# Kernel optimization log

Hardware: AMD Instinct MI355X
Metric: run time of the kernel (lower is better)

Reference implementation:

```python
import jax, jax.numpy as jnp
import numpy as np

B, N, L = 32, 50, 16384  # batch, n_templates, segment length
KT = 4096                # template kernel length


def conv1d(x, w, pad, groups=1):
    # x: [B, Cin, L], w: [Cout, Cin/groups, K] (torch layout)
    return jax.lax.conv_general_dilated(
        x, w, window_strides=(1,), padding=[(pad, pad)],
        dimension_numbers=('NCH', 'OIH', 'NCH'), feature_group_count=groups)


def maxpool3(x):
    # MaxPool1d(kernel=3, stride=3), floor mode (VALID)
    return jax.lax.reduce_window(x, -jnp.inf, jax.lax.max,
                                 (1, 1, 3), (1, 1, 3), 'VALID')


def pad_to(x, m):
    p = (-x.shape[-1]) % m
    pads = ((0, 0),) * (x.ndim - 1) + ((0, p),)
    return jnp.pad(x, pads)


def setup_inputs() -> dict:
    key = jax.random.key(0)
    ks = jax.random.split(key, 12)
    return dict(
        xi=jax.random.normal(ks[0], (B, 2, L), jnp.float32),
        S_t_m12=jax.random.normal(ks[1], (2, 1, L), jnp.float32) * 0.01,
        template=jax.random.normal(ks[2], (N, 2, KT), jnp.float32) * 0.01,
        hh_sqrt=jax.random.uniform(ks[3], (N, 2), jnp.float32) + 0.5,
        W1=jax.random.normal(ks[4], (16, 2, 3), jnp.float32) * 0.1,
        b1=jnp.zeros((16,), jnp.float32),
        W2=jax.random.normal(ks[5], (32, 16, 3), jnp.float32) * 0.1,
        b2=jnp.zeros((32,), jnp.float32),
        W3=jax.random.normal(ks[6], (32, 128), jnp.float32) * 0.1,
        b3=jnp.zeros((32,), jnp.float32),
        W4=jax.random.normal(ks[7], (2, 32), jnp.float32) * 0.1,
        b4=jnp.zeros((2,), jnp.float32),
    )


def reference(xi, S_t_m12, template, hh_sqrt, W1, b1, W2, b2, W3, b3, W4, b4):
    # Whitening matched filter: grouped conv with kernel length L
    y = conv1d(xi, S_t_m12, L - 1, groups=2)          # [B, 2, 2L-1]
    y = pad_to(y, L)                                   # [B, 2, 2L]
    # wrap-fold each channel: reshape(B,2,L).sum over the fold axis
    d_SA = y[:, 0].reshape(-1, 2, L).sum(1)[:, None, :]  # [B,1,L]
    d_SE = y[:, 1].reshape(-1, 2, L).sum(1)[:, None, :]
    h_SA = template[:, 0, :].reshape(-1, 1, KT)          # [N,1,KT]
    h_SE = template[:, 1, :].reshape(-1, 1, KT)
    dh_A = pad_to(conv1d(d_SA, h_SA, KT - 1), L).reshape(-1, N, 2, L).sum(2)  # [B,N,L]
    dh_E = pad_to(conv1d(d_SE, h_SE, KT - 1), L).reshape(-1, N, 2, L).sum(2)
    z = jnp.stack((dh_A, dh_E), -1).transpose(0, 2, 1, 3)  # [B,L,N,2]
    z = z / hh_sqrt                                         # broadcast [N,2]
    z = z.max(axis=1).transpose(0, 2, 1)                    # [B,2,N]
    # small CNN + MLP head
    h = maxpool3(jax.nn.sigmoid(conv1d(z, W1, 0) + b1[None, :, None]))  # [B,16,16]
    h = maxpool3(jax.nn.sigmoid(conv1d(h, W2, 0) + b2[None, :, None]))  # [B,32,4]
    h = h.reshape(h.shape[0], -1)                                        # [B,128]
    h = jax.nn.relu(h @ W3.T + b3)
    return h @ W4.T + b4                                                 # [B,2]
```

## Files before the change

kernel.cpp:

```cpp
#include <hip/hip_runtime.h>
#include <math.h>

#define L_LEN 16384
#define M_LEN 8192
#define KT_LEN 4096
#define BB 32
#define NTPL 50
#define SPEC_STRIDE 8224
#define NSIG 166
#define NTI 512
#define PI_F 3.14159265358979323846f
#define R2_F 0.70710678118654752f
#define CW1 0.99999970586288223f
#define SW1 7.6699031874270453e-4f

typedef float cf2 __attribute__((ext_vector_type(2)));


__device__ __forceinline__ cf2 cmul(cf2 a, cf2 b) {
    cf2 t, d;
    asm("v_pk_mul_f32 %0, %1, %2 op_sel:[0,0] op_sel_hi:[0,1]"
        : "=v"(t) : "v"(a), "v"(b));
    asm("v_pk_fma_f32 %0, %1, %2, %3 op_sel:[1,1,0] op_sel_hi:[1,0,1] neg_lo:[0,1,0]"
        : "=v"(d) : "v"(a), "v"(b), "v"(t));
    return d;
}
__device__ __forceinline__ cf2 cmulc(cf2 a, cf2 b) {
    cf2 t, d;
    asm("v_pk_mul_f32 %0, %1, %2 op_sel:[0,0] op_sel_hi:[0,1] neg_hi:[0,1]"
        : "=v"(t) : "v"(a), "v"(b));
    asm("v_pk_fma_f32 %0, %1, %2, %3 op_sel:[1,1,0] op_sel_hi:[1,0,1]"
        : "=v"(d) : "v"(a), "v"(b), "v"(t));
    return d;
}
__device__ __forceinline__ cf2 cmulca(cf2 a, cf2 b) {
    cf2 t, d;
    asm("v_pk_mul_f32 %0, %1, %2 op_sel:[0,0] op_sel_hi:[0,1]"
        : "=v"(t) : "v"(a), "v"(b));
    asm("v_pk_fma_f32 %0, %1, %2, %3 op_sel:[1,1,0] op_sel_hi:[1,0,1] neg_hi:[1,0,0]"
        : "=v"(d) : "v"(a), "v"(b), "v"(t));
    return d;
}
__device__ __forceinline__ cf2 pk_addch(cf2 a, cf2 b) {
    cf2 d;
    asm("v_pk_add_f32 %0, %1, %2 neg_hi:[0,1]" : "=v"(d) : "v"(a), "v"(b));
    return d;
}
__device__ __forceinline__ cf2 pk_subcl(cf2 a, cf2 b) {
    cf2 d;
    asm("v_pk_add_f32 %0, %1, %2 neg_lo:[0,1]" : "=v"(d) : "v"(a), "v"(b));
    return d;
}
__device__ __forceinline__ cf2 pk_compose1(cf2 s, cf2 r) {
    cf2 d;
    asm("v_pk_add_f32 %0, %1, %2 op_sel:[0,1] op_sel_hi:[0,0] neg_lo:[0,1]"
        : "=v"(d) : "v"(s), "v"(r));
    return d;
}
__device__ __forceinline__ cf2 pk_compose2(cf2 s, cf2 r) {
    cf2 d;
    asm("v_pk_add_f32 %0, %1, %2 op_sel:[0,1] op_sel_hi:[0,0] neg_hi:[1,0]"
        : "=v"(d) : "v"(s), "v"(r));
    return d;
}
template<int SIGN>
__device__ __forceinline__ cf2 rot90(cf2 z) {
    return (SIGN < 0) ? (cf2){z.y, -z.x} : (cf2){-z.y, z.x};
}
template<int SIGN>
__device__ __forceinline__ cf2 ldT(const cf2* __restrict__ T, int idx) {
    cf2 t = T[idx];
    if (SIGN > 0) t.y = -t.y;
    return t;
}

__device__ __forceinline__ int swz(int i) { return i ^ (((i >> 5) & 15) << 1); }

__device__ __forceinline__ int pos4(int f) {
    return ((f & 15) << 8) | (f & 0xF0) | ((f >> 8) & 15);
}

template<int SIGN>
__device__ __forceinline__ void dft16(cf2 x[16]) {
    const float S = (SIGN < 0) ? -1.f : 1.f;
    const cf2 w1 = {0.9238795325112867f, S * 0.3826834323650898f};
    const cf2 w2 = {0.7071067811865476f, S * 0.7071067811865476f};
    const cf2 w3 = {0.3826834323650898f, S * 0.9238795325112867f};
    cf2 v[16];
    #pragma unroll
    for (int n1 = 0; n1 < 4; ++n1) {
        cf2 a0 = x[n1], a1 = x[n1+4], a2 = x[n1+8], a3 = x[n1+12];
        cf2 t0 = a0 + a2, t2 = a0 - a2;
        cf2 t1 = a1 + a3, t3 = rot90<SIGN>(a1 - a3);
        cf2 u0 = t0 + t1, u1 = t2 + t3;
        cf2 u2 = t0 - t1, u3 = t2 - t3;
        if (n1 == 1) { u1 = cmul(u1, w1); u2 = cmul(u2, w2); u3 = cmul(u3, w3); }
        else if (n1 == 2) { u1 = cmul(u1, w2); u2 = rot90<SIGN>(u2);
                            u3 = rot90<SIGN>(cmul(u3, w2)); }
        else if (n1 == 3) { u1 = cmul(u1, w3); u2 = rot90<SIGN>(cmul(u2, w2));
                            u3 = -cmul(u3, w1); }
        v[0*4+n1] = u0; v[1*4+n1] = u1; v[2*4+n1] = u2; v[3*4+n1] = u3;
    }
    #pragma unroll
    for (int r = 0; r < 4; ++r) {
        cf2 a0 = v[r*4+0], a1 = v[r*4+1], a2 = v[r*4+2], a3 = v[r*4+3];
        cf2 t0 = a0 + a2, t2 = a0 - a2;
        cf2 t1 = a1 + a3, t3 = rot90<SIGN>(a1 - a3);
        x[r]    = t0 + t1; x[r+4]  = t2 + t3;
        x[r+8]  = t0 - t1; x[r+12] = t2 - t3;
    }
}

template<int SIGN>
__device__ __forceinline__ void butterfly16(cf2* A, const int idx[16], cf2 w1) {
    cf2 x[16];
    #pragma unroll
    for (int n = 0; n < 16; ++n) x[n] = A[idx[n]];
    dft16<SIGN>(x);
    A[idx[0]] = x[0];
    A[idx[1]] = cmul(x[1], w1);
    const cf2 w2 = cmul(w1, w1);
    A[idx[2]] = cmul(x[2], w2);
    const cf2 w3 = cmul(w1, w2);
    A[idx[3]] = cmul(x[3], w3);
    const cf2 w4 = cmul(w2, w2);
    A[idx[4]] = cmul(x[4], w4);
    A[idx[5]] = cmul(x[5], cmul(w1, w4));
    A[idx[6]] = cmul(x[6], cmul(w2, w4));
    A[idx[7]] = cmul(x[7], cmul(w3, w4));
    const cf2 w8 = cmul(w4, w4);
    A[idx[8]]  = cmul(x[8],  w8);
    A[idx[9]]  = cmul(x[9],  cmul(w1, w8));
    A[idx[10]] = cmul(x[10], cmul(w2, w8));
    A[idx[11]] = cmul(x[11], cmul(w3, w8));
    const cf2 w12 = cmul(w4, w8);
    A[idx[12]] = cmul(x[12], w12);
    A[idx[13]] = cmul(x[13], cmul(w1, w12));
    A[idx[14]] = cmul(x[14], cmul(w2, w12));
    A[idx[15]] = cmul(x[15], cmul(w3, w12));
}

__global__ __launch_bounds__(256, 4)
void fwd_fft_kernel(const float* __restrict__ xi, const float* __restrict__ w,
                    const float* __restrict__ tmpl, cf2* __restrict__ Tw,
                    cf2* __restrict__ spec) {
    __shared__ __attribute__((aligned(16))) cf2 A[4096];
    const int hb = blockIdx.x;
    const int tid = threadIdx.x;

    if (hb >= 2*NSIG) {
        const int k = (hb - 2*NSIG) * 256 + tid;
        const int quad = k >> 12, mm = k & 4095;
        float s, c; __sincosf(PI_F * (float)mm / 8192.f, &s, &c);
        cf2 v;
        if      (quad == 0) v = (cf2){ c, -s};
        else if (quad == 1) v = (cf2){-s, -c};
        else if (quad == 2) v = (cf2){-c,  s};
        else                v = (cf2){ s,  c};
        Tw[k] = v;
        return;
    }

    const int sig = hb >> 1, half = hb & 1;
    const float* src;
    int nre;
    if (sig < 64)      { src = xi   + sig * L_LEN;         nre = L_LEN; }
    else if (sig < 66) { src = w    + (sig - 64) * L_LEN;  nre = L_LEN; }
    else               { src = tmpl + (sig - 66) * KT_LEN; nre = KT_LEN; }
    const bool isW = (sig >= 64 && sig < 66);
    const int nf4 = nre >> 2;
    const float4* s4 = (const float4*)src;

    const cf2 w1c = (cf2){CW1, -SW1};
    #pragma unroll
    for (int mm = 0; mm < 8; ++mm) {
        const int j = tid + 256*mm;
        float4 a = (j < nf4)        ? s4[j]        : make_float4(0.f,0.f,0.f,0.f);
        float4 b = (j + 2048 < nf4) ? s4[j + 2048] : make_float4(0.f,0.f,0.f,0.f);
        cf2 c0 = (cf2){a.x, a.y}, c1 = (cf2){a.z, a.w};
        cf2 d0 = (cf2){b.x, b.y}, d1 = (cf2){b.z, b.w};
        cf2 h0, h1;
        if (half == 0) { h0 = c0 + d0; h1 = c1 + d1; }
        else {
            float sn, cs; __sincosf(-PI_F * (float)j / 2048.f, &sn, &cs);
            cf2 wk = (cf2){cs, sn};
            h0 = cmul(c0 - d0, wk);
            h1 = cmul(c1 - d1, cmul(wk, w1c));
        }
        const int g = j ^ ((j >> 4) & 15);
        ((float4*)A)[g] = make_float4(h0.x, h0.y, h1.x, h1.y);
    }
    __syncthreads();

    {
        const int jx = tid ^ (((tid >> 5) & 7) << 1);
        int idx[16];
        #pragma unroll
        for (int n = 0; n < 16; ++n) idx[n] = (jx ^ ((n & 1) << 4)) + 256*n;
        float sn, cs; __sincosf(-PI_F * (float)tid / 2048.f, &sn, &cs);
        butterfly16<-1>(A, idx, (cf2){cs, sn});
    }
    __syncthreads();
    {
        const int q = tid >> 4, j = tid & 15;
        const int base = q << 8, qb = q & 1;
        int idx[16];
        #pragma unroll
        for (int n = 0; n < 16; ++n)
            idx[n] = base + 16*(n ^ qb) + (j ^ (((n >> 1) & 7) << 1));
        float sn, cs; __sincosf(-PI_F * (float)j / 128.f, &sn, &cs);
        butterfly16<-1>(A, idx, (cf2){cs, sn});
    }
    __syncthreads();
    {
        const int bb = 16 * (tid ^ ((tid >> 4) & 1));
        const int m3 = ((tid >> 1) & 7) << 1;
        cf2 x[16];
        #pragma unroll
        for (int e = 0; e < 8; ++e) {
            float4 v = ((const float4*)A)[(bb + ((2*e) ^ m3)) >> 1];
            x[2*e]     = (cf2){v.x, v.y};
            x[2*e + 1] = (cf2){v.z, v.w};
        }
        dft16<-1>(x);
        #pragma unroll
        for (int e = 0; e < 8; ++e)
            ((float4*)A)[(bb + ((2*e) ^ m3)) >> 1] =
                make_float4(x[2*e].x, x[2*e].y, x[2*e+1].x, x[2*e+1].y);
    }
    __syncthreads();

    cf2* out = spec + (size_t)sig * SPEC_STRIDE;
    #pragma unroll
    for (int mm = 0; mm < 16; ++mm) {
        const int m = tid + 256*mm;
        const int mb = half ? (4095 - m) : ((4096 - m) & 4095);
        const int f = 2*m + half;
        cf2 Za = A[swz(pos4(m))];
        cf2 Zb = A[swz(pos4(mb))];
        cf2 E = (cf2){0.5f*(Za.x + Zb.x), 0.5f*(Za.y - Zb.y)};
        cf2 D = (cf2){Za.x - Zb.x, Za.y + Zb.y};
        cf2 O = (cf2){0.5f*D.y, -0.5f*D.x};
        float sn, cs;
        __sincosf(-PI_F * (float)f / 8192.f, &sn, &cs);
        cf2 val = E + (cf2){cs*O.x - sn*O.y, cs*O.y + sn*O.x};
        if (isW) {
            const int k = (4094 * f) & (L_LEN - 1);
            float psn, pcs; __sincosf(-PI_F * (float)k / 8192.f, &psn, &pcs);
            val = cmul((cf2){val.x, -val.y}, (cf2){pcs, psn});
        }
        out[f] = val;
    }
    if (half == 0 && tid == 0) {
        cf2 Za = A[0];
        cf2 val = (cf2){Za.x - Za.y, 0.f};
        if (isW) {
            val = (cf2){-val.x, 0.f};
        }
        out[M_LEN] = val;
    }
}

__global__ __launch_bounds__(1024)
void xv_kernel(cf2* __restrict__ spec) {
    const int bc = blockIdx.x;
    cf2* Xs = spec + (size_t)bc * SPEC_STRIDE;
    const cf2* Vs = spec + (size_t)(64 + (bc & 1)) * SPEC_STRIDE;
    const int tid = threadIdx.x;
    float4* X4 = (float4*)Xs;
    const float4* V4 = (const float4*)Vs;
    #pragma unroll
    for (int m = 0; m < 4; ++m) {
        const int p = tid + 1024*m;
        float4 xv = X4[p], vv = V4[p];
        cf2 a = cmul((cf2){xv.x, xv.y}, (cf2){vv.x, vv.y});
        cf2 b = cmul((cf2){xv.z, xv.w}, (cf2){vv.z, vv.w});
        X4[p] = make_float4(a.x, a.y, b.x, b.y);
    }
    if (tid == 0) Xs[M_LEN] = cmul(Xs[M_LEN], Vs[M_LEN]);
}

__global__ __launch_bounds__(NTI, 4)
void inv_fft_kernel(const cf2* __restrict__ spec, const cf2* __restrict__ T,
                    const float* __restrict__ hh, float* __restrict__ zarr) {
    __shared__ __attribute__((aligned(16))) cf2 A[M_LEN];
    const int idx0 = blockIdx.x;
    const int c = idx0 & 1;
    const int n = (idx0 >> 1) % NTPL;
    const int b = idx0 / (2 * NTPL);
    const int tid = threadIdx.x;

    const cf2* Xs = spec + (size_t)(b*2 + c)      * SPEC_STRIDE;
    const cf2* Hs = spec + (size_t)(66 + n*2 + c) * SPEC_STRIDE;
    const float4* X4 = (const float4*)Xs;
    const float4* H4 = (const float4*)Hs;
    const float4* T4 = (const float4*)T;

    #pragma unroll
    for (int m = 0; m < 2; ++m) {
        const int tp = tid + 512*m;
        const int f0 = 2*tp, f1 = f0 + 1;
        float4 xa = X4[tp],        ha = H4[tp];
        float4 xq = X4[tp + 2048], hq = H4[tp + 2048];
        cf2 PA0 = cmulc((cf2){xa.x, xa.y}, (cf2){ha.x, ha.y});
        cf2 PA1 = cmulc((cf2){xa.z, xa.w}, (cf2){ha.z, ha.w});
        cf2 QB0 = cmulc((cf2){xq.x, xq.y}, (cf2){hq.x, hq.y});
        cf2 QB1 = cmulc((cf2){xq.z, xq.w}, (cf2){hq.z, hq.w});
        cf2 PB0 = cmulc(Xs[4096 - f0], Hs[4096 - f0]);
        cf2 PB1 = cmulc(Xs[4096 - f1], Hs[4096 - f1]);
        cf2 QA0 = cmulc(Xs[8192 - f0], Hs[8192 - f0]);
        cf2 QA1 = cmulc(Xs[8192 - f1], Hs[8192 - f1]);
        float4 tf4 = T4[tp];
        float4 t2a = T4[2*tp];
        float4 t2b = T4[2*tp + 1];
        cf2 Tf0 = (cf2){tf4.x, tf4.y}, Tf1 = (cf2){tf4.z, tf4.w};
        cf2 T20 = (cf2){t2a.x, t2a.y}, T21 = (cf2){t2b.x, t2b.y};
        cf2 SpA0 = pk_addch(PA0, QA0), SmA0 = pk_subcl(PA0, QA0);
        cf2 RA0 = cmulca(Tf0, SmA0);
        cf2 ZA1_0 = pk_compose1(SpA0, RA0);
        cf2 ZA2_0 = pk_compose2(SpA0, RA0);
        cf2 tB0 = (cf2){-Tf0.y, -Tf0.x};
        cf2 SpB0 = pk_addch(PB0, QB0), SmB0 = pk_subcl(PB0, QB0);
        cf2 RB0 = cmulca(tB0, SmB0);
        cf2 ZB1_0 = pk_compose1(SpB0, RB0);
        cf2 ZB2_0 = pk_compose2(SpB0, RB0);
        cf2 top0 = ZA1_0 + ZB2_0;
        cf2 bot0 = cmulca(T20, ZA1_0 - ZB2_0);
        cf2 SpA1 = pk_addch(PA1, QA1), SmA1 = pk_subcl(PA1, QA1);
        cf2 RA1 = cmulca(Tf1, SmA1);
        cf2 ZA1_1 = pk_compose1(SpA1, RA1);
        cf2 ZA2_1 = pk_compose2(SpA1, RA1);
        cf2 tB1 = (cf2){-Tf1.y, -Tf1.x};
        cf2 SpB1 = pk_addch(PB1, QB1), SmB1 = pk_subcl(PB1, QB1);
        cf2 RB1 = cmulca(tB1, SmB1);
        cf2 ZB1_1 = pk_compose1(SpB1, RB1);
        cf2 ZB2_1 = pk_compose2(SpB1, RB1);
        cf2 top1 = ZA1_1 + ZB2_1;
        cf2 bot1 = cmulca(T21, ZA1_1 - ZB2_1);
        const int gt = tp ^ ((tp >> 4) & 15);
        ((float4*)A)[gt]        = make_float4(top0.x, top0.y, top1.x, top1.y);
        ((float4*)A)[2048 + gt] = make_float4(bot0.x, bot0.y, bot1.x, bot1.y);
        if (tp > 0) {
            cf2 tr0 = ZB1_0 + ZA2_0;
            cf2 dr0 = cmul(ZB1_0 - ZA2_0, T20);
            A[swz(4096 - f0)] = tr0;
            A[swz(8192 - f0)] = -dr0;
        }
        cf2 tr1 = ZB1_1 + ZA2_1;
        cf2 dr1 = cmul(ZB1_1 - ZA2_1, T21);
        A[swz(4096 - f1)] = tr1;
        A[swz(8192 - f1)] = -dr1;
    }
    if (tid == 0) {
        cf2 P = cmulc(Xs[2048], Hs[2048]);
        cf2 Q = cmulc(Xs[6144], Hs[6144]);
        cf2 Tc = (cf2){R2_F, -R2_F};
        cf2 Sp = pk_addch(P, Q), Sm = pk_subcl(P, Q);
        cf2 R = cmulca(Tc, Sm);
        cf2 Z1 = pk_compose1(Sp, R), Z2 = pk_compose2(Sp, R);
        cf2 d = Z1 - Z2;
        A[swz(2048)] = Z1 + Z2;
        A[swz(6144)] = (cf2){-d.y, d.x};
    }
    __syncthreads();

    {
        const int h = tid >> 8, j = tid & 255;
        const int Hb = h << 12;
        const int jx = j ^ (((j >> 5) & 7) << 1);
        int idx[16];
        #pragma unroll
        for (int nn = 0; nn < 16; ++nn)
            idx[nn] = Hb + 256*nn + (jx ^ ((nn & 1) << 4));
        butterfly16<+1>(A, idx, ldT<+1>(T, 4*j));
    }
    __syncthreads();
    {
        const int h = tid >> 8, q = (tid >> 4) & 15, j = tid & 15;
        const int base = (h << 12) + (q << 8);
        const int qb = q & 1;
        int idx[16];
        #pragma unroll
        for (int nn = 0; nn < 16; ++nn)
            idx[nn] = base + 16*(nn ^ qb) + (j ^ (((nn >> 1) & 7) << 1));
        butterfly16<+1>(A, idx, ldT<+1>(T, 64*j));
    }
    __syncthreads();

    float mx = -INFINITY;
    {
        const int bb = 16 * (tid ^ ((tid >> 4) & 1));
        const int m3 = ((tid >> 1) & 7) << 1;
        cf2 x[16];
        #pragma unroll
        for (int e = 0; e < 8; ++e) {
            float4 v = ((const float4*)A)[(bb + ((2*e) ^ m3)) >> 1];
            x[2*e]     = (cf2){v.x, v.y};
            x[2*e + 1] = (cf2){v.z, v.w};
        }
        dft16<+1>(x);
        #pragma unroll
        for (int nn = 0; nn < 16; ++nn)
            mx = fmaxf(mx, fmaxf(x[nn].x, x[nn].y));
    }
    __syncthreads();
    for (int off = 32; off > 0; off >>= 1)
        mx = fmaxf(mx, __shfl_xor(mx, off));
    const int lane = tid & 63, wv = tid >> 6;
    float* redf = (float*)A;
    if (lane == 0) redf[wv] = mx;
    __syncthreads();
    if (tid == 0) {
        float mm = redf[0];
        for (int i = 1; i < NTI/64; ++i) mm = fmaxf(mm, redf[i]);
        zarr[(b*2 + c)*NTPL + n] = mm / (2.f * (float)M_LEN * hh[n*2 + c]);
    }
}

#define W1_OFF 0
#define B1_OFF 96
#define W2_OFF 112
#define B2_OFF 1648
#define W3_OFF 1680
#define B3_OFF 5904
#define W4_OFF 5936
#define B4_OFF 6000
#define WSM_SZ 6002

__global__ __launch_bounds__(256)
void head_kernel(const float* __restrict__ zarr,
                 const float* __restrict__ W1, const float* __restrict__ b1,
                 const float* __restrict__ W2, const float* __restrict__ b2,
                 const float* __restrict__ W3, const float* __restrict__ b3,
                 const float* __restrict__ W4, const float* __restrict__ b4,
                 float* __restrict__ out) {
    __shared__ float wsm[WSM_SZ];
    __shared__ float zl[2*NTPL];
    __shared__ float s1[16*48];
    __shared__ float p1[16*16];
    __shared__ float s2[32*14];
    __shared__ float hflat[128];
    __shared__ float h1[32];
    const int b = blockIdx.x, tid = threadIdx.x;

    for (int i = tid; i < 96;   i += 256) wsm[W1_OFF + i] = W1[i];
    if (tid < 16)                         wsm[B1_OFF + tid] = b1[tid];
    for (int i = tid; i < 1536; i += 256) wsm[W2_OFF + i] = W2[i];
    if (tid < 32)                         wsm[B2_OFF + tid] = b2[tid];
    for (int i = tid; i < 4096; i += 256)
        wsm[W3_OFF + (i >> 7)*132 + (i & 127)] = W3[i];
    if (tid < 32)                         wsm[B3_OFF + tid] = b3[tid];
    if (tid < 64)                         wsm[W4_OFF + tid] = W4[tid];
    if (tid < 2)                          wsm[B4_OFF + tid] = b4[tid];
    for (int i = tid; i < 2*NTPL; i += 256) zl[i] = zarr[b*2*NTPL + i];
    __syncthreads();

    for (int i = tid; i < 16*48; i += 256) {
        const int o = i / 48, t = i % 48;
        float acc = wsm[B1_OFF + o];
        #pragma unroll
        for (int cc = 0; cc < 2; ++cc)
            #pragma unroll
            for (int k = 0; k < 3; ++k)
                acc += zl[cc*NTPL + t + k] * wsm[W1_OFF + o*6 + cc*3 + k];
        s1[i] = 1.f / (1.f + __expf(-acc));
    }
    __syncthreads();
    for (int i = tid; i < 16*16; i += 256) {
        const int o = i / 16, u = i % 16;
        p1[i] = fmaxf(fmaxf(s1[o*48 + 3*u], s1[o*48 + 3*u+1]), s1[o*48 + 3*u+2]);
    }
    __syncthreads();
    for (int i = tid; i < 32*14; i += 256) {
        const int o = i / 14, t = i % 14;
        float acc = wsm[B2_OFF + o];
        #pragma unroll
        for (int cc = 0; cc < 16; ++cc)
            #pragma unroll
            for (int k = 0; k < 3; ++k)
                acc += p1[cc*16 + t + k] * wsm[W2_OFF + o*48 + cc*3 + k];
        s2[o*14 + t] = 1.f / (1.f + __expf(-acc));
    }
    __syncthreads();
    for (int i = tid; i < 128; i += 256) {
        const int o = i / 4, u = i % 4;
        hflat[i] = fmaxf(fmaxf(s2[o*14 + 3*u], s2[o*14 + 3*u+1]), s2[o*14 + 3*u+2]);
    }
    __syncthreads();
    {
        const int o = tid >> 3, lg = tid & 7;
        float acc = 0.f;
        #pragma unroll
        for (int k = 0; k < 16; ++k)
            acc += hflat[lg + 8*k] * wsm[W3_OFF + o*132 + lg + 8*k];
        acc += __shfl_xor(acc, 1);
        acc += __shfl_xor(acc, 2);
        acc += __shfl_xor(acc, 4);
        if (lg == 0) h1[o] = fmaxf(acc + wsm[B3_OFF + o], 0.f);
    }
    __syncthreads();
    if (tid < 64) {
        const int o = tid >> 5, j = tid & 31;
        float p = h1[j] * wsm[W4_OFF + o*32 + j];
        p += __shfl_xor(p, 1);
        p += __shfl_xor(p, 2);
        p += __shfl_xor(p, 4);
        p += __shfl_xor(p, 8);
        p += __shfl_xor(p, 16);
        if (j == 0) out[b*2 + o] = p + wsm[B4_OFF + o];
    }
}

extern "C" void kernel_launch(void* const* d_in, const int* in_sizes, int n_in,
                              void* d_out, int out_size, void* d_ws, size_t ws_size,
                              hipStream_t stream) {
    const float* xi   = (const float*)d_in[0];
    const float* Sw   = (const float*)d_in[1];
    const float* tmpl = (const float*)d_in[2];
    const float* hh   = (const float*)d_in[3];
    const float* W1   = (const float*)d_in[4];
    const float* b1   = (const float*)d_in[5];
    const float* W2   = (const float*)d_in[6];
    const float* b2   = (const float*)d_in[7];
    const float* W3   = (const float*)d_in[8];
    const float* b3   = (const float*)d_in[9];
    const float* W4   = (const float*)d_in[10];
    const float* b4   = (const float*)d_in[11];
    float* out = (float*)d_out;

    cf2* T16  = (cf2*)d_ws;
    cf2* spec = T16 + 16384;
    float* zarr = (float*)(spec + (size_t)NSIG * SPEC_STRIDE);

    fwd_fft_kernel<<<dim3(2*NSIG + 64), dim3(256), 0, stream>>>(xi, Sw, tmpl, T16, spec);
    xv_kernel<<<dim3(64), dim3(1024), 0, stream>>>(spec);
    inv_fft_kernel<<<dim3(BB * NTPL * 2), dim3(NTI), 0, stream>>>(spec, T16, hh, zarr);
    head_kernel<<<dim3(BB), dim3(256), 0, stream>>>(zarr, W1, b1, W2, b2, W3, b3, W4, b4, out);
}
```

Baseline: 155.4 us.

## Store even/odd spectrum halves contiguously and widen forward FFT blocks

The forward FFT now writes even and odd frequency bins into two contiguous half-arrays (odd half at a fixed offset) instead of interleaving them. This lets each forward block write coalesced output and lets the inverse kernel read both halves contiguously. The forward kernel also grows to 512 threads so loads and stores are spread wider, though only 256 threads do the butterfly stages and the rest sit idle there. The pointwise multiply and inverse-kernel indexing are rewritten to match the new layout.

```diff
diff --git a/kernel.cpp b/kernel.cpp
--- a/kernel.cpp
+++ b/kernel.cpp
@@ -7,7 +7,9 @@
 #define BB 32
 #define NTPL 50
 #define SPEC_STRIDE 8224
+#define OOFF 4112
 #define NSIG 166
+#define NTFH 512
 #define NTI 512
 #define PI_F 3.14159265358979323846f
 #define R2_F 0.70710678118654752f
@@ -140,7 +142,7 @@
     A[idx[15]] = cmul(x[15], cmul(w3, w12));
 }
 
-__global__ __launch_bounds__(256, 4)
+__global__ __launch_bounds__(NTFH, 4)
 void fwd_fft_kernel(const float* __restrict__ xi, const float* __restrict__ w,
                     const float* __restrict__ tmpl, cf2* __restrict__ Tw,
                     cf2* __restrict__ spec) {
@@ -149,7 +151,7 @@
     const int tid = threadIdx.x;
 
     if (hb >= 2*NSIG) {
-        const int k = (hb - 2*NSIG) * 256 + tid;
+        const int k = (hb - 2*NSIG) * NTFH + tid;
         const int quad = k >> 12, mm = k & 4095;
         float s, c; __sincosf(PI_F * (float)mm / 8192.f, &s, &c);
         cf2 v;
@@ -173,8 +175,8 @@
 
     const cf2 w1c = (cf2){CW1, -SW1};
     #pragma unroll
-    for (int mm = 0; mm < 8; ++mm) {
-        const int j = tid + 256*mm;
+    for (int mm = 0; mm < 4; ++mm) {
+        const int j = tid + 512*mm;
         float4 a = (j < nf4)        ? s4[j]        : make_float4(0.f,0.f,0.f,0.f);
         float4 b = (j + 2048 < nf4) ? s4[j + 2048] : make_float4(0.f,0.f,0.f,0.f);
         cf2 c0 = (cf2){a.x, a.y}, c1 = (cf2){a.z, a.w};
@@ -192,7 +194,7 @@
     }
     __syncthreads();
 
-    {
+    if (tid < 256) {
         const int jx = tid ^ (((tid >> 5) & 7) << 1);
         int idx[16];
         #pragma unroll
@@ -201,7 +203,7 @@
         butterfly16<-1>(A, idx, (cf2){cs, sn});
     }
     __syncthreads();
-    {
+    if (tid < 256) {
         const int q = tid >> 4, j = tid & 15;
         const int base = q << 8, qb = q & 1;
         int idx[16];
@@ -212,7 +214,7 @@
         butterfly16<-1>(A, idx, (cf2){cs, sn});
     }
     __syncthreads();
-    {
+    if (tid < 256) {
         const int bb = 16 * (tid ^ ((tid >> 4) & 1));
         const int m3 = ((tid >> 1) & 7) << 1;
         cf2 x[16];
@@ -230,10 +232,10 @@
     }
     __syncthreads();
 
-    cf2* out = spec + (size_t)sig * SPEC_STRIDE;
-    #pragma unroll
-    for (int mm = 0; mm < 16; ++mm) {
-        const int m = tid + 256*mm;
+    cf2* outh = spec + (size_t)sig * SPEC_STRIDE + (half ? OOFF : 0);
+    #pragma unroll
+    for (int mm = 0; mm < 8; ++mm) {
+        const int m = tid + 512*mm;
         const int mb = half ? (4095 - m) : ((4096 - m) & 4095);
         const int f = 2*m + half;
         cf2 Za = A[swz(pos4(m))];
@@ -249,15 +251,13 @@
             float psn, pcs; __sincosf(-PI_F * (float)k / 8192.f, &psn, &pcs);
             val = cmul((cf2){val.x, -val.y}, (cf2){pcs, psn});
         }
-        out[f] = val;
+        outh[m] = val;
     }
     if (half == 0 && tid == 0) {
         cf2 Za = A[0];
         cf2 val = (cf2){Za.x - Za.y, 0.f};
-        if (isW) {
-            val = (cf2){-val.x, 0.f};
-        }
-        out[M_LEN] = val;
+        if (isW) val = (cf2){-val.x, 0.f};
+        outh[4096] = val;
     }
 }
 
@@ -270,14 +270,22 @@
     float4* X4 = (float4*)Xs;
     const float4* V4 = (const float4*)Vs;
     #pragma unroll
-    for (int m = 0; m < 4; ++m) {
+    for (int m = 0; m < 2; ++m) {
         const int p = tid + 1024*m;
         float4 xv = X4[p], vv = V4[p];
         cf2 a = cmul((cf2){xv.x, xv.y}, (cf2){vv.x, vv.y});
         cf2 b = cmul((cf2){xv.z, xv.w}, (cf2){vv.z, vv.w});
         X4[p] = make_float4(a.x, a.y, b.x, b.y);
     }
-    if (tid == 0) Xs[M_LEN] = cmul(Xs[M_LEN], Vs[M_LEN]);
+    #pragma unroll
+    for (int m = 0; m < 2; ++m) {
+        const int p = 2056 + tid + 1024*m;
+        float4 xv = X4[p], vv = V4[p];
+        cf2 a = cmul((cf2){xv.x, xv.y}, (cf2){vv.x, vv.y});
+        cf2 b = cmul((cf2){xv.z, xv.w}, (cf2){vv.z, vv.w});
+        X4[p] = make_float4(a.x, a.y, b.x, b.y);
+    }
+    if (tid == 0) Xs[4096] = cmul(Xs[4096], Vs[4096]);
 }
 
 __global__ __launch_bounds__(NTI, 4)
@@ -290,26 +298,24 @@
     const int b = idx0 / (2 * NTPL);
     const int tid = threadIdx.x;
 
-    const cf2* Xs = spec + (size_t)(b*2 + c)      * SPEC_STRIDE;
-    const cf2* Hs = spec + (size_t)(66 + n*2 + c) * SPEC_STRIDE;
-    const float4* X4 = (const float4*)Xs;
-    const float4* H4 = (const float4*)Hs;
+    const cf2* Xe = spec + (size_t)(b*2 + c)      * SPEC_STRIDE;
+    const cf2* He = spec + (size_t)(66 + n*2 + c) * SPEC_STRIDE;
+    const cf2* Xo = Xe + OOFF;
+    const cf2* Ho = He + OOFF;
     const float4* T4 = (const float4*)T;
 
     #pragma unroll
     for (int m = 0; m < 2; ++m) {
         const int tp = tid + 512*m;
-        const int f0 = 2*tp, f1 = f0 + 1;
-        float4 xa = X4[tp],        ha = H4[tp];
-        float4 xq = X4[tp + 2048], hq = H4[tp + 2048];
-        cf2 PA0 = cmulc((cf2){xa.x, xa.y}, (cf2){ha.x, ha.y});
-        cf2 PA1 = cmulc((cf2){xa.z, xa.w}, (cf2){ha.z, ha.w});
-        cf2 QB0 = cmulc((cf2){xq.x, xq.y}, (cf2){hq.x, hq.y});
-        cf2 QB1 = cmulc((cf2){xq.z, xq.w}, (cf2){hq.z, hq.w});
-        cf2 PB0 = cmulc(Xs[4096 - f0], Hs[4096 - f0]);
-        cf2 PB1 = cmulc(Xs[4096 - f1], Hs[4096 - f1]);
-        cf2 QA0 = cmulc(Xs[8192 - f0], Hs[8192 - f0]);
-        cf2 QA1 = cmulc(Xs[8192 - f1], Hs[8192 - f1]);
+        cf2 PA0 = cmulc(Xe[tp],        He[tp]);
+        cf2 PA1 = cmulc(Xo[tp],        Ho[tp]);
+        cf2 QB0 = cmulc(Xe[2048 + tp], He[2048 + tp]);
+        cf2 QB1 = cmulc(Xo[2048 + tp], Ho[2048 + tp]);
+        cf2 PB0 = cmulc(Xe[2048 - tp], He[2048 - tp]);
+        cf2 PB1 = cmulc(Xo[2047 - tp], Ho[2047 - tp]);
+        cf2 QA0 = cmulc(Xe[4096 - tp], He[4096 - tp]);
+        cf2 QA1 = cmulc(Xo[4095 - tp], Ho[4095 - tp]);
+        const int f0 = 2*tp;
         float4 tf4 = T4[tp];
         float4 t2a = T4[2*tp];
         float4 t2b = T4[2*tp + 1];
@@ -348,12 +354,12 @@
         }
         cf2 tr1 = ZB1_1 + ZA2_1;
         cf2 dr1 = cmul(ZB1_1 - ZA2_1, T21);
-        A[swz(4096 - f1)] = tr1;
-        A[swz(8192 - f1)] = -dr1;
+        A[swz(4096 - f0 - 1)] = tr1;
+        A[swz(8192 - f0 - 1)] = -dr1;
     }
     if (tid == 0) {
-        cf2 P = cmulc(Xs[2048], Hs[2048]);
-        cf2 Q = cmulc(Xs[6144], Hs[6144]);
+        cf2 P = cmulc(Xe[1024], He[1024]);
+        cf2 Q = cmulc(Xe[3072], He[3072]);
         cf2 Tc = (cf2){R2_F, -R2_F};
         cf2 Sp = pk_addch(P, Q), Sm = pk_subcl(P, Q);
         cf2 R = cmulca(Tc, Sm);
@@ -532,7 +538,7 @@
     cf2* spec = T16 + 16384;
     float* zarr = (float*)(spec + (size_t)NSIG * SPEC_STRIDE);
 
-    fwd_fft_kernel<<<dim3(2*NSIG + 64), dim3(256), 0, stream>>>(xi, Sw, tmpl, T16, spec);
+    fwd_fft_kernel<<<dim3(2*NSIG + 32), dim3(NTFH), 0, stream>>>(xi, Sw, tmpl, T16, spec);
     xv_kernel<<<dim3(64), dim3(1024), 0, stream>>>(spec);
     inv_fft_kernel<<<dim3(BB * NTPL * 2), dim3(NTI), 0, stream>>>(spec, T16, hh, zarr);
     head_kernel<<<dim3(BB), dim3(256), 0, stream>>>(zarr, W1, b1, W2, b2, W3, b3, W4, b4, out);
```

After: 155.2 us. Within noise of the previous version (-0.1%).
